# Kernel optimization log

Measured on AMD Instinct MI355X. Metric: run time of the kernel, lower is better.

## Reference

```python
import jax, jax.numpy as jnp
import numpy as np

B, T, Dx, H, K = 32, 4096, 128, 128, 10


def setup_inputs() -> dict:
    key = jax.random.key(0)
    ks = jax.random.split(key, 11)
    s = 1.0 / np.sqrt(H)  # PyTorch GRU init range

    def p(k, shape):
        return jax.random.uniform(k, shape, jnp.float32, -s, s)

    return {
        "x": jax.random.normal(ks[0], (B, T, Dx), jnp.float32),
        # forward-direction GRU params (gate order: r, z, n as in PyTorch)
        "W_ih_f": p(ks[1], (3 * H, Dx)),
        "W_hh_f": p(ks[2], (3 * H, H)),
        "b_ih_f": p(ks[3], (3 * H,)),
        "b_hh_f": p(ks[4], (3 * H,)),
        # backward-direction GRU params
        "W_ih_b": p(ks[5], (3 * H, Dx)),
        "W_hh_b": p(ks[6], (3 * H, H)),
        "b_ih_b": p(ks[7], (3 * H,)),
        "b_hh_b": p(ks[8], (3 * H,)),
        # final linear classifier
        "W_fc": p(ks[9], (K, 2 * H)),
        "b_fc": p(ks[10], (K,)),
    }


def _gru_scan(x, Wih, Whh, bih, bhh, reverse):
    """Single-direction GRU over time. x: [B,T,Dx] -> [B,T,H]."""
    # Precompute all input projections at once: [T, B, 3H]
    xp = jnp.einsum('btd,gd->tbg', x, Wih) + bih
    Whh_T = Whh.T
    Hd = Whh.shape[1]

    def cell(h, xt):
        hp = h @ Whh_T + bhh            # [B, 3H]
        xr, xz, xn = jnp.split(xt, 3, axis=-1)
        hr, hz, hn = jnp.split(hp, 3, axis=-1)
        r = jax.nn.sigmoid(xr + hr)
        z = jax.nn.sigmoid(xz + hz)
        n = jnp.tanh(xn + r * hn)
        h_new = (1.0 - z) * n + z * h
        return h_new, h_new

    h0 = jnp.zeros((x.shape[0], Hd), x.dtype)
    _, hs = jax.lax.scan(cell, h0, xp, reverse=reverse)  # [T, B, H]
    return jnp.transpose(hs, (1, 0, 2))


def reference(x, W_ih_f, W_hh_f, b_ih_f, b_hh_f,
              W_ih_b, W_hh_b, b_ih_b, b_hh_b, W_fc, b_fc):
    hf = _gru_scan(x, W_ih_f, W_hh_f, b_ih_f, b_hh_f, reverse=False)
    hb = _gru_scan(x, W_ih_b, W_hh_b, b_ih_b, b_hh_b, reverse=True)
    h = jnp.concatenate([hf, hb], axis=-1)  # [B, T, 2H]
    return h @ W_fc.T + b_fc                # [B, T, K]
```

## Files before the change

kernel.cpp:

```cpp
#include <hip/hip_runtime.h>
#include <cstdint>
#include <cstddef>

#define T_LEN   4096
#define B_SZ    32
#define H_DIM   128
#define DX      128
#define K_CLS   10
#define CHUNK   32
#define NCHUNKS (T_LEN / CHUNK)
#define XA_LD   136
#define XP_LD   408
#define HI_LD   136

typedef _Float16 half8   __attribute__((ext_vector_type(8)));
typedef float    floatx4 __attribute__((ext_vector_type(4)));

__device__ __forceinline__ float sigm(float x) {
  x = fminf(fmaxf(x, -30.f), 30.f);
  return __builtin_amdgcn_rcpf(1.f + __expf(-x));
}

__device__ __forceinline__ float tanhfast(float x) {
  x = fminf(fmaxf(x, -15.f), 15.f);
  float t = __expf(-2.f * x);
  return (1.f - t) * __builtin_amdgcn_rcpf(1.f + t);
}

__global__ void __launch_bounds__(256) init_out_kernel(float* __restrict__ out,
                                                       const float* __restrict__ bfc) {
  int i = blockIdx.x * 256 + threadIdx.x;
  if (i < B_SZ * T_LEN * K_CLS) out[i] = bfc[i % K_CLS];
}

__global__ void __launch_bounds__(512, 2)
gru_bidir_kernel(const float* __restrict__ x,
                 const float* __restrict__ Wih_f, const float* __restrict__ Whh_f,
                 const float* __restrict__ bih_f, const float* __restrict__ bhh_f,
                 const float* __restrict__ Wih_b, const float* __restrict__ Whh_b,
                 const float* __restrict__ bih_b, const float* __restrict__ bhh_b,
                 const float* __restrict__ Wfc, float* __restrict__ out) {
  const int tid = threadIdx.x;
  const int bid = blockIdx.x;
  const int b   = bid & (B_SZ - 1);
  const int dir = bid >> 5;

  const float* Wih = dir ? Wih_b : Wih_f;
  const float* Whh = dir ? Whh_b : Whh_f;
  const float* bih = dir ? bih_b : bih_f;
  const float* bhh = dir ? bhh_b : bhh_f;

  const int lane = tid & 63;
  const int wv   = tid >> 6;
  const int col  = lane & 15;
  const int quad = lane >> 4;
  const int jloc = wv * 16 + col;

  __shared__ __align__(16) _Float16 xA[CHUNK][XA_LD];
  __shared__ __align__(16) _Float16 xPL[CHUNK][XP_LD];
  __shared__ __align__(16) _Float16 hist[CHUNK + 1][HI_LD];

  half8 whf[3][4];
  half8 wif[3][4];
#pragma unroll
  for (int g = 0; g < 3; ++g) {
#pragma unroll
    for (int kt = 0; kt < 4; ++kt) {
      const float* sh = Whh + (size_t)(g * H_DIM + jloc) * H_DIM + kt * 32 + quad * 8;
      const float* si = Wih + (size_t)(g * H_DIM + jloc) * DX + kt * 32 + quad * 8;
      half8 vh, vi;
#pragma unroll
      for (int e = 0; e < 8; ++e) {
        vh[e] = (_Float16)sh[e];
        vi[e] = (_Float16)si[e];
      }
      whf[g][kt] = vh;
      wif[g][kt] = vi;
    }
  }
  const float bias_r = bih[jloc] + bhh[jloc];
  const float bias_z = bih[H_DIM + jloc] + bhh[H_DIM + jloc];
  const float bias_n = bih[2 * H_DIM + jloc];
  const float bhn    = bhh[2 * H_DIM + jloc];

  half8 fcf[4];
  if (wv < 2) {
#pragma unroll
    for (int kt = 0; kt < 4; ++kt) {
      half8 v;
#pragma unroll
      for (int e = 0; e < 8; ++e) {
        int k = kt * 32 + quad * 8 + e;
        v[e] = (col < K_CLS) ? (_Float16)Wfc[(size_t)col * (2 * H_DIM) + dir * H_DIM + k]
                             : (_Float16)0.f;
      }
      fcf[kt] = v;
    }
  }

  half8 hz;
#pragma unroll
  for (int e = 0; e < 8; ++e) hz[e] = (_Float16)0.f;
  half8 haf0 = hz, haf1 = hz, haf2 = hz, haf3 = hz;

  if (tid < H_DIM) hist[0][tid] = (_Float16)0.f;

  const int s_row = tid >> 4;
  const int cb    = (tid & 15) * 8;
  float4 px0, px1;
  {
    int t0 = dir ? (T_LEN - 1 - s_row) : s_row;
    const float* xr = x + ((size_t)b * T_LEN + t0) * DX + cb;
    px0 = *(const float4*)xr;
    px1 = *(const float4*)(xr + 4);
  }

  float hold = 0.f;
  const floatx4 z4 = {0.f, 0.f, 0.f, 0.f};
  __syncthreads();

  for (int c = 0; c < NCHUNKS; ++c) {
    {
      half8 v;
      v[0] = (_Float16)px0.x; v[1] = (_Float16)px0.y; v[2] = (_Float16)px0.z; v[3] = (_Float16)px0.w;
      v[4] = (_Float16)px1.x; v[5] = (_Float16)px1.y; v[6] = (_Float16)px1.z; v[7] = (_Float16)px1.w;
      *(half8*)&xA[s_row][cb] = v;
    }
    __syncthreads();

#pragma unroll
    for (int mt = 0; mt < 2; ++mt) {
      half8 af[4];
#pragma unroll
      for (int kt = 0; kt < 4; ++kt)
        af[kt] = *(const half8*)&xA[mt * 16 + col][kt * 32 + quad * 8];
#pragma unroll
      for (int g = 0; g < 3; ++g) {
        floatx4 a = z4;
#pragma unroll
        for (int kt = 0; kt < 4; ++kt)
          a = __builtin_amdgcn_mfma_f32_16x16x32_f16(af[kt], wif[g][kt], a, 0, 0, 0);
        float bb = (g == 0) ? bias_r : (g == 1) ? bias_z : bias_n;
#pragma unroll
        for (int i = 0; i < 4; ++i)
          xPL[mt * 16 + quad * 4 + i][g * H_DIM + jloc] = (_Float16)(a[i] + bb);
      }
    }

    if (c + 1 < NCHUNKS) {
      int s  = (c + 1) * CHUNK + s_row;
      int t0 = dir ? (T_LEN - 1 - s) : s;
      const float* xr = x + ((size_t)b * T_LEN + t0) * DX + cb;
      px0 = *(const float4*)xr;
      px1 = *(const float4*)(xr + 4);
    }
    __syncthreads();

#pragma unroll 2
    for (int s = 0; s < CHUNK; ++s) {
      if (col == 0) {
        haf0 = *(const half8*)&hist[s][quad * 8];
        haf1 = *(const half8*)&hist[s][32 + quad * 8];
        haf2 = *(const half8*)&hist[s][64 + quad * 8];
        haf3 = *(const half8*)&hist[s][96 + quad * 8];
      }
      floatx4 arA = __builtin_amdgcn_mfma_f32_16x16x32_f16(haf0, whf[0][0], z4, 0, 0, 0);
      arA = __builtin_amdgcn_mfma_f32_16x16x32_f16(haf1, whf[0][1], arA, 0, 0, 0);
      floatx4 arB = __builtin_amdgcn_mfma_f32_16x16x32_f16(haf2, whf[0][2], z4, 0, 0, 0);
      arB = __builtin_amdgcn_mfma_f32_16x16x32_f16(haf3, whf[0][3], arB, 0, 0, 0);

      floatx4 azA = __builtin_amdgcn_mfma_f32_16x16x32_f16(haf0, whf[1][0], z4, 0, 0, 0);
      azA = __builtin_amdgcn_mfma_f32_16x16x32_f16(haf1, whf[1][1], azA, 0, 0, 0);
      floatx4 azB = __builtin_amdgcn_mfma_f32_16x16x32_f16(haf2, whf[1][2], z4, 0, 0, 0);
      azB = __builtin_amdgcn_mfma_f32_16x16x32_f16(haf3, whf[1][3], azB, 0, 0, 0);

      floatx4 anA = __builtin_amdgcn_mfma_f32_16x16x32_f16(haf0, whf[2][0], z4, 0, 0, 0);
      anA = __builtin_amdgcn_mfma_f32_16x16x32_f16(haf1, whf[2][1], anA, 0, 0, 0);
      floatx4 anB = __builtin_amdgcn_mfma_f32_16x16x32_f16(haf2, whf[2][2], z4, 0, 0, 0);
      anB = __builtin_amdgcn_mfma_f32_16x16x32_f16(haf3, whf[2][3], anB, 0, 0, 0);

      float ar = arA[0] + arB[0];
      float az = azA[0] + azB[0];
      float an = anA[0] + anB[0];

      float xr = (float)xPL[s][jloc];
      float xz = (float)xPL[s][H_DIM + jloc];
      float xn = (float)xPL[s][2 * H_DIM + jloc];

      float rr = sigm(xr + ar);
      float zz = sigm(xz + az);
      float nn = tanhfast(xn + rr * (an + bhn));
      hold = nn + zz * (hold - nn);

      if (quad == 0) hist[s + 1][jloc] = (_Float16)hold;
      __syncthreads();
    }

    if (wv < 2) {
      floatx4 fa = z4;
#pragma unroll
      for (int kt = 0; kt < 4; ++kt) {
        half8 af = *(const half8*)&hist[1 + wv * 16 + col][kt * 32 + quad * 8];
        fa = __builtin_amdgcn_mfma_f32_16x16x32_f16(af, fcf[kt], fa, 0, 0, 0);
      }
      if (col < K_CLS) {
#pragma unroll
        for (int i = 0; i < 4; ++i) {
          int t  = c * CHUNK + wv * 16 + quad * 4 + i;
          int tt = dir ? (T_LEN - 1 - t) : t;
          atomicAdd(out + ((size_t)b * T_LEN + tt) * K_CLS + col, fa[i]);
        }
      }
    }
    if (tid >= 256 && tid < 256 + H_DIM) hist[0][tid - 256] = hist[CHUNK][tid - 256];
  }
}

extern "C" void kernel_launch(void* const* d_in, const int* in_sizes, int n_in,
                              void* d_out, int out_size, void* d_ws, size_t ws_size,
                              hipStream_t stream) {
  (void)in_sizes; (void)n_in; (void)d_ws; (void)ws_size; (void)out_size;
  const float* x     = (const float*)d_in[0];
  const float* Wih_f = (const float*)d_in[1];
  const float* Whh_f = (const float*)d_in[2];
  const float* bih_f = (const float*)d_in[3];
  const float* bhh_f = (const float*)d_in[4];
  const float* Wih_b = (const float*)d_in[5];
  const float* Whh_b = (const float*)d_in[6];
  const float* bih_b = (const float*)d_in[7];
  const float* bhh_b = (const float*)d_in[8];
  const float* Wfc   = (const float*)d_in[9];
  const float* bfc   = (const float*)d_in[10];
  float* out = (float*)d_out;

  const int n_out = B_SZ * T_LEN * K_CLS;
  init_out_kernel<<<(n_out + 255) / 256, 256, 0, stream>>>(out, bfc);
  gru_bidir_kernel<<<B_SZ * 2, 512, 0, stream>>>(x, Wih_f, Whh_f, bih_f, bhh_f,
                                                 Wih_b, Whh_b, bih_b, bhh_b, Wfc, out);
}
```

Baseline: 1.810 ms.

## Prescale GRU weights by log2e, interleave gate projections, shorten serial step

Weights and biases are prescaled by log2(e) (and by 2·log2(e) for the n gate), so the activations can call exp2 directly without extra multiplies or clamps. The precomputed input projections are stored interleaved as r,z,n,pad per hidden unit, so each step reads them with one 8-byte LDS load that is prefetched one step ahead. The recurrent MFMAs become 12 independent ops with no accumulator chaining, which shortens the dependency chain. __syncthreads is replaced by an lgkmcnt wait plus s_barrier. The fp16 rounding of the prescaled weights shifts numerics slightly, and the larger XP_LD increases LDS use.

```diff
diff --git a/kernel.cpp b/kernel.cpp
--- a/kernel.cpp
+++ b/kernel.cpp
@@ -10,22 +10,19 @@
 #define CHUNK   32
 #define NCHUNKS (T_LEN / CHUNK)
 #define XA_LD   136
-#define XP_LD   408
+#define XP_LD   520
 #define HI_LD   136
 
+typedef _Float16 half2v  __attribute__((ext_vector_type(2)));
+typedef _Float16 half4   __attribute__((ext_vector_type(4)));
 typedef _Float16 half8   __attribute__((ext_vector_type(8)));
 typedef float    floatx4 __attribute__((ext_vector_type(4)));
 
-__device__ __forceinline__ float sigm(float x) {
-  x = fminf(fmaxf(x, -30.f), 30.f);
-  return __builtin_amdgcn_rcpf(1.f + __expf(-x));
-}
-
-__device__ __forceinline__ float tanhfast(float x) {
-  x = fminf(fmaxf(x, -15.f), 15.f);
-  float t = __expf(-2.f * x);
-  return (1.f - t) * __builtin_amdgcn_rcpf(1.f + t);
-}
+#define LGKM_BARRIER() do {                                   \
+    asm volatile("s_waitcnt lgkmcnt(0)" ::: "memory");        \
+    __builtin_amdgcn_s_barrier();                             \
+    asm volatile("" ::: "memory");                            \
+  } while (0)
 
 __global__ void __launch_bounds__(256) init_out_kernel(float* __restrict__ out,
                                                        const float* __restrict__ bfc) {
@@ -60,10 +57,13 @@
   __shared__ __align__(16) _Float16 xPL[CHUNK][XP_LD];
   __shared__ __align__(16) _Float16 hist[CHUNK + 1][HI_LD];
 
+  const float LOG2E = 1.44269504f;
+
   half8 whf[3][4];
   half8 wif[3][4];
 #pragma unroll
   for (int g = 0; g < 3; ++g) {
+    const float gs = (g == 2) ? 2.0f * LOG2E : LOG2E;
 #pragma unroll
     for (int kt = 0; kt < 4; ++kt) {
       const float* sh = Whh + (size_t)(g * H_DIM + jloc) * H_DIM + kt * 32 + quad * 8;
@@ -71,17 +71,17 @@
       half8 vh, vi;
 #pragma unroll
       for (int e = 0; e < 8; ++e) {
-        vh[e] = (_Float16)sh[e];
-        vi[e] = (_Float16)si[e];
+        vh[e] = (_Float16)(sh[e] * gs);
+        vi[e] = (_Float16)(si[e] * gs);
       }
       whf[g][kt] = vh;
       wif[g][kt] = vi;
     }
   }
-  const float bias_r = bih[jloc] + bhh[jloc];
-  const float bias_z = bih[H_DIM + jloc] + bhh[H_DIM + jloc];
-  const float bias_n = bih[2 * H_DIM + jloc];
-  const float bhn    = bhh[2 * H_DIM + jloc];
+  const float bias_r = (bih[jloc] + bhh[jloc]) * LOG2E;
+  const float bias_z = (bih[H_DIM + jloc] + bhh[H_DIM + jloc]) * LOG2E;
+  const float bias_n = bih[2 * H_DIM + jloc] * (2.0f * LOG2E);
+  const float bhn_s  = bhh[2 * H_DIM + jloc] * (2.0f * LOG2E);
 
   half8 fcf[4];
   if (wv < 2) {
@@ -126,7 +126,7 @@
       v[4] = (_Float16)px1.x; v[5] = (_Float16)px1.y; v[6] = (_Float16)px1.z; v[7] = (_Float16)px1.w;
       *(half8*)&xA[s_row][cb] = v;
     }
-    __syncthreads();
+    LGKM_BARRIER();
 
 #pragma unroll
     for (int mt = 0; mt < 2; ++mt) {
@@ -134,16 +134,21 @@
 #pragma unroll
       for (int kt = 0; kt < 4; ++kt)
         af[kt] = *(const half8*)&xA[mt * 16 + col][kt * 32 + quad * 8];
-#pragma unroll
-      for (int g = 0; g < 3; ++g) {
-        floatx4 a = z4;
-#pragma unroll
-        for (int kt = 0; kt < 4; ++kt)
-          a = __builtin_amdgcn_mfma_f32_16x16x32_f16(af[kt], wif[g][kt], a, 0, 0, 0);
-        float bb = (g == 0) ? bias_r : (g == 1) ? bias_z : bias_n;
-#pragma unroll
-        for (int i = 0; i < 4; ++i)
-          xPL[mt * 16 + quad * 4 + i][g * H_DIM + jloc] = (_Float16)(a[i] + bb);
+      floatx4 pr = z4, pz = z4, pn = z4;
+#pragma unroll
+      for (int kt = 0; kt < 4; ++kt) {
+        pr = __builtin_amdgcn_mfma_f32_16x16x32_f16(af[kt], wif[0][kt], pr, 0, 0, 0);
+        pz = __builtin_amdgcn_mfma_f32_16x16x32_f16(af[kt], wif[1][kt], pz, 0, 0, 0);
+        pn = __builtin_amdgcn_mfma_f32_16x16x32_f16(af[kt], wif[2][kt], pn, 0, 0, 0);
+      }
+#pragma unroll
+      for (int i = 0; i < 4; ++i) {
+        half4 w;
+        w[0] = (_Float16)(pr[i] + bias_r);
+        w[1] = (_Float16)(pz[i] + bias_z);
+        w[2] = (_Float16)(pn[i] + bias_n);
+        w[3] = (_Float16)0.f;
+        *(half4*)&xPL[mt * 16 + quad * 4 + i][jloc * 4] = w;
       }
     }
 
@@ -154,7 +159,9 @@
       px0 = *(const float4*)xr;
       px1 = *(const float4*)(xr + 4);
     }
-    __syncthreads();
+    LGKM_BARRIER();
+
+    uint2 xv = *(const uint2*)&xPL[0][jloc * 4];
 
 #pragma unroll 2
     for (int s = 0; s < CHUNK; ++s) {
@@ -164,36 +171,38 @@
         haf2 = *(const half8*)&hist[s][64 + quad * 8];
         haf3 = *(const half8*)&hist[s][96 + quad * 8];
       }
-      floatx4 arA = __builtin_amdgcn_mfma_f32_16x16x32_f16(haf0, whf[0][0], z4, 0, 0, 0);
-      arA = __builtin_amdgcn_mfma_f32_16x16x32_f16(haf1, whf[0][1], arA, 0, 0, 0);
-      floatx4 arB = __builtin_amdgcn_mfma_f32_16x16x32_f16(haf2, whf[0][2], z4, 0, 0, 0);
-      arB = __builtin_amdgcn_mfma_f32_16x16x32_f16(haf3, whf[0][3], arB, 0, 0, 0);
-
-      floatx4 azA = __builtin_amdgcn_mfma_f32_16x16x32_f16(haf0, whf[1][0], z4, 0, 0, 0);
-      azA = __builtin_amdgcn_mfma_f32_16x16x32_f16(haf1, whf[1][1], azA, 0, 0, 0);
-      floatx4 azB = __builtin_amdgcn_mfma_f32_16x16x32_f16(haf2, whf[1][2], z4, 0, 0, 0);
-      azB = __builtin_amdgcn_mfma_f32_16x16x32_f16(haf3, whf[1][3], azB, 0, 0, 0);
-
-      floatx4 anA = __builtin_amdgcn_mfma_f32_16x16x32_f16(haf0, whf[2][0], z4, 0, 0, 0);
-      anA = __builtin_amdgcn_mfma_f32_16x16x32_f16(haf1, whf[2][1], anA, 0, 0, 0);
-      floatx4 anB = __builtin_amdgcn_mfma_f32_16x16x32_f16(haf2, whf[2][2], z4, 0, 0, 0);
-      anB = __builtin_amdgcn_mfma_f32_16x16x32_f16(haf3, whf[2][3], anB, 0, 0, 0);
-
-      float ar = arA[0] + arB[0];
-      float az = azA[0] + azB[0];
-      float an = anA[0] + anB[0];
-
-      float xr = (float)xPL[s][jloc];
-      float xz = (float)xPL[s][H_DIM + jloc];
-      float xn = (float)xPL[s][2 * H_DIM + jloc];
-
-      float rr = sigm(xr + ar);
-      float zz = sigm(xz + az);
-      float nn = tanhfast(xn + rr * (an + bhn));
+      uint2 xvn = *(const uint2*)&xPL[(s + 1) & (CHUNK - 1)][jloc * 4];
+
+      floatx4 cr0 = __builtin_amdgcn_mfma_f32_16x16x32_f16(haf0, whf[0][0], z4, 0, 0, 0);
+      floatx4 cr1 = __builtin_amdgcn_mfma_f32_16x16x32_f16(haf1, whf[0][1], z4, 0, 0, 0);
+      floatx4 cr2 = __builtin_amdgcn_mfma_f32_16x16x32_f16(haf2, whf[0][2], z4, 0, 0, 0);
+      floatx4 cr3 = __builtin_amdgcn_mfma_f32_16x16x32_f16(haf3, whf[0][3], z4, 0, 0, 0);
+      floatx4 cz0 = __builtin_amdgcn_mfma_f32_16x16x32_f16(haf0, whf[1][0], z4, 0, 0, 0);
+      floatx4 cz1 = __builtin_amdgcn_mfma_f32_16x16x32_f16(haf1, whf[1][1], z4, 0, 0, 0);
+      floatx4 cz2 = __builtin_amdgcn_mfma_f32_16x16x32_f16(haf2, whf[1][2], z4, 0, 0, 0);
+      floatx4 cz3 = __builtin_amdgcn_mfma_f32_16x16x32_f16(haf3, whf[1][3], z4, 0, 0, 0);
+      floatx4 cn0 = __builtin_amdgcn_mfma_f32_16x16x32_f16(haf0, whf[2][0], z4, 0, 0, 0);
+      floatx4 cn1 = __builtin_amdgcn_mfma_f32_16x16x32_f16(haf1, whf[2][1], z4, 0, 0, 0);
+      floatx4 cn2 = __builtin_amdgcn_mfma_f32_16x16x32_f16(haf2, whf[2][2], z4, 0, 0, 0);
+      floatx4 cn3 = __builtin_amdgcn_mfma_f32_16x16x32_f16(haf3, whf[2][3], z4, 0, 0, 0);
+
+      float ar = (cr0[0] + cr1[0]) + (cr2[0] + cr3[0]);
+      float az = (cz0[0] + cz1[0]) + (cz2[0] + cz3[0]);
+      float an = (cn0[0] + cn1[0]) + (cn2[0] + cn3[0]);
+
+      half2v x01 = __builtin_bit_cast(half2v, xv.x);
+      half2v x23 = __builtin_bit_cast(half2v, xv.y);
+
+      float rr = __builtin_amdgcn_rcpf(1.f + __builtin_amdgcn_exp2f(-((float)x01.x + ar)));
+      float zz = __builtin_amdgcn_rcpf(1.f + __builtin_amdgcn_exp2f(-((float)x01.y + az)));
+      float yn = fmaf(rr, an + bhn_s, (float)x23.x);
+      float t  = __builtin_amdgcn_exp2f(-fmaxf(yn, -80.f));
+      float nn = (1.f - t) * __builtin_amdgcn_rcpf(1.f + t);
       hold = nn + zz * (hold - nn);
 
       if (quad == 0) hist[s + 1][jloc] = (_Float16)hold;
-      __syncthreads();
+      LGKM_BARRIER();
+      xv = xvn;
     }
 
     if (wv < 2) {
```

Measured after the change: 1.724 ms. -4.7%, faster.
